# Kernel tuning notes

Measured on AMD Instinct MI355X. Metric: run time of the kernel, lower is better.

The kernel has to match this reference:

```python
import math
import jax, jax.numpy as jnp
import numpy as np

DIM = 256
B = 32
M = 2048
N = 2048


def setup_inputs() -> dict:
    key = jax.random.key(0)
    k1, k2, k3, k4 = jax.random.split(key, 4)
    query = jax.random.normal(k1, (B, DIM, M), dtype=jnp.float32)
    key_t = jax.random.normal(k2, (B, DIM, N), dtype=jnp.float32)
    value = jax.random.normal(k3, (B, DIM, N), dtype=jnp.float32)
    # orthogonal random projection via QR, as in the torch __init__
    proj = np.asarray(jax.random.normal(k4, (DIM, DIM), dtype=jnp.float32))
    orth_proj, _ = np.linalg.qr(proj)
    orth_proj = jnp.asarray(orth_proj, dtype=jnp.float32)
    return {"query": query, "key": key_t, "value": value, "orth_proj": orth_proj}


def reference(query, key, value, orth_proj):
    dim = orth_proj.shape[0]
    q = query / math.sqrt(dim)
    # kernel feature maps: relu(W^T x), channels-first layout b c m
    phi_q = jax.nn.relu(jnp.einsum('bcm,ce->bem', q, orth_proj))
    phi_k = jax.nn.relu(jnp.einsum('bcn,ce->ben', key, orth_proj))
    phi_k_rowsum = phi_k.sum(-1)                         # [b, e]
    scale = jnp.einsum('bem,be->bm', phi_q, phi_k_rowsum)  # [b, m]
    scale = 1.0 / (scale + 1e-8)
    phi_q = phi_q * scale[:, None, :]                    # [b, e, m]
    kv = jnp.einsum('ben,bdn->bed', phi_k, value)        # [b, e, d]
    out = jnp.einsum('bem,bed->bdm', phi_q, kv)          # [b, d, m]
    return out
```

## Files before the change

### kernel.cpp

```cpp
#include <hip/hip_runtime.h>

#define DIMC 256
#define BSZ  32
#define MDIM 2048
#define NDIM 2048

#define KVP_STRIDE ((size_t)BSZ * DIMC * DIMC)

typedef __attribute__((ext_vector_type(8))) short bf16x8;
typedef __attribute__((ext_vector_type(4))) float f32x4;

static __device__ __forceinline__ unsigned short f2bf(float x) {
  unsigned int u = __float_as_uint(x);
  u += 0x7fffu + ((u >> 16) & 1u);
  return (unsigned short)(u >> 16);
}
static __device__ __forceinline__ float bf2f(unsigned short h) {
  return __uint_as_float(((unsigned int)h) << 16);
}
static __device__ __forceinline__ unsigned int cvt_pk_bf16(float lo, float hi) {
  unsigned int r;
  asm("v_cvt_pk_bf16_f32 %0, %1, %2" : "=v"(r) : "v"(lo), "v"(hi));
  return r;
}

__global__ __launch_bounds__(256) void prep_kernel(
    const float* __restrict__ W, unsigned short* __restrict__ Wt,
    float* __restrict__ rowsum) {
  const int e = blockIdx.x, c = threadIdx.x;
  Wt[e * 256 + c] = f2bf(W[c * 256 + e]);
  if (e < 32) rowsum[e * 256 + c] = 0.f;
}

__global__ __launch_bounds__(256) void phi_kernel(
    const float* __restrict__ query, const float* __restrict__ key,
    const unsigned short* __restrict__ Wt,
    unsigned short* __restrict__ phi_q, unsigned short* __restrict__ phi_k,
    float* __restrict__ rowsum) {
  __shared__ unsigned short As[128 * 40];
  __shared__ unsigned short Bs[128 * 40];
  const int z = blockIdx.z;
  const bool isKey = z < BSZ;
  const int b = isKey ? z : z - BSZ;
  const int x0 = blockIdx.x * 128;
  const int e0 = blockIdx.y * 128;
  const int t = threadIdx.x;
  const int lane = t & 63, wave = t >> 6;
  const int wr = wave >> 1, wc = wave & 1;
  const int q = lane >> 4, l15 = lane & 15;
  const float* Xb =
      (isKey ? key : query) + (size_t)b * DIMC * NDIM;
  f32x4 acc[4][4];
#pragma unroll
  for (int i = 0; i < 4; ++i)
#pragma unroll
    for (int j = 0; j < 4; ++j) acc[i][j] = (f32x4){0.f, 0.f, 0.f, 0.f};

  const int arow = t >> 2, ac8 = (t & 3) << 3;
  const int xidx = t & 127, ch = (t >> 7) << 4;
  const float* src0 = Xb + (size_t)ch * NDIM + x0 + xidx;
  const unsigned short* wt0 = Wt + (size_t)(e0 + arow) * 256 + ac8;
  const unsigned short* wt1 = Wt + (size_t)(e0 + arow + 64) * 256 + ac8;

  float v[16];
#pragma unroll
  for (int i = 0; i < 16; ++i) v[i] = src0[(size_t)i * NDIM];
  uint4 w0 = *(const uint4*)wt0;
  uint4 w1 = *(const uint4*)wt1;

  for (int it = 0; it < 8; ++it) {
    const int k0 = it * 32;
    {
      unsigned int wpk[8];
#pragma unroll
      for (int i = 0; i < 8; ++i) wpk[i] = cvt_pk_bf16(v[2 * i], v[2 * i + 1]);
      *(uint4*)&Bs[xidx * 40 + ch] = *(const uint4*)&wpk[0];
      *(uint4*)&Bs[xidx * 40 + ch + 8] = *(const uint4*)&wpk[4];
      *(uint4*)&As[arow * 40 + ac8] = w0;
      *(uint4*)&As[(arow + 64) * 40 + ac8] = w1;
    }
    __syncthreads();
    if (it < 7) {
      const float* src = src0 + (size_t)(k0 + 32) * NDIM;
#pragma unroll
      for (int i = 0; i < 16; ++i) v[i] = src[(size_t)i * NDIM];
      w0 = *(const uint4*)(wt0 + k0 + 32);
      w1 = *(const uint4*)(wt1 + k0 + 32);
    }
    bf16x8 a[4], bv[4];
#pragma unroll
    for (int i = 0; i < 4; ++i)
      a[i] = *(const bf16x8*)&As[(wr * 64 + i * 16 + l15) * 40 + q * 8];
#pragma unroll
    for (int j = 0; j < 4; ++j)
      bv[j] = *(const bf16x8*)&Bs[(wc * 64 + j * 16 + l15) * 40 + q * 8];
#pragma unroll
    for (int i = 0; i < 4; ++i)
#pragma unroll
      for (int j = 0; j < 4; ++j)
        acc[i][j] =
            __builtin_amdgcn_mfma_f32_16x16x32_bf16(a[i], bv[j], acc[i][j], 0, 0, 0);
    __syncthreads();
  }

  if (isKey) {
    unsigned short* dst = phi_k + (size_t)b * DIMC * NDIM;
#pragma unroll
    for (int i = 0; i < 4; ++i)
#pragma unroll
      for (int r = 0; r < 4; ++r) {
        const int e = e0 + wr * 64 + i * 16 + q * 4 + r;
        float s = 0.f;
#pragma unroll
        for (int j = 0; j < 4; ++j) {
          float vv = acc[i][j][r];
          vv = vv > 0.f ? vv : 0.f;
          const int n = x0 + wc * 64 + j * 16 + l15;
          dst[(size_t)e * NDIM + n] = f2bf(vv);
          s += vv;
        }
#pragma unroll
        for (int m = 1; m < 16; m <<= 1) s += __shfl_xor(s, m, 64);
        if (l15 == 0) atomicAdd(&rowsum[b * DIMC + e], s);
      }
  } else {
    unsigned short* dst = phi_q + (size_t)b * MDIM * DIMC;
#pragma unroll
    for (int i = 0; i < 4; ++i) {
      const int ebase = e0 + wr * 64 + i * 16 + q * 4;
#pragma unroll
      for (int j = 0; j < 4; ++j) {
        const int m = x0 + wc * 64 + j * 16 + l15;
        float r0 = acc[i][j][0], r1 = acc[i][j][1];
        float r2 = acc[i][j][2], r3 = acc[i][j][3];
        r0 = r0 > 0.f ? r0 * 0.0625f : 0.f;
        r1 = r1 > 0.f ? r1 * 0.0625f : 0.f;
        r2 = r2 > 0.f ? r2 * 0.0625f : 0.f;
        r3 = r3 > 0.f ? r3 * 0.0625f : 0.f;
        uint2 p;
        p.x = cvt_pk_bf16(r0, r1);
        p.y = cvt_pk_bf16(r2, r3);
        *(uint2*)&dst[(size_t)m * DIMC + ebase] = p;
      }
    }
  }
}

__global__ __launch_bounds__(256) void kv_kernel(
    const float* __restrict__ value, const unsigned short* __restrict__ phi_k,
    unsigned short* __restrict__ kvp, int kshift) {
  __shared__ unsigned short As[128 * 72];
  __shared__ unsigned short Bs[128 * 72];
  const int b = blockIdx.z >> kshift, ks = blockIdx.z & ((1 << kshift) - 1);
  const int d0 = blockIdx.x * 128, e0 = blockIdx.y * 128;
  const int t = threadIdx.x;
  const int lane = t & 63, wave = t >> 6;
  const int wr = wave >> 1, wc = wave & 1;
  const int q = lane >> 4, l15 = lane & 15;
  f32x4 acc[4][4];
#pragma unroll
  for (int i = 0; i < 4; ++i)
#pragma unroll
    for (int j = 0; j < 4; ++j) acc[i][j] = (f32x4){0.f, 0.f, 0.f, 0.f};

  const int row = t >> 2;
  const int c4 = (t & 3) << 2;
  const int c8 = (t & 3) << 3;

  const float* asrc0 = value + ((size_t)b * DIMC + d0 + row) * NDIM;
  const float* asrc1 = asrc0 + (size_t)64 * NDIM;
  const unsigned short* bsrc0 = phi_k + ((size_t)b * DIMC + e0 + row) * NDIM;
  const unsigned short* bsrc1 = bsrc0 + (size_t)64 * NDIM;

  const int nchunk = NDIM >> kshift;
  const int nbeg = ks * nchunk;
  for (int n0 = nbeg; n0 < nbeg + nchunk; n0 += 64) {
    __syncthreads();
#pragma unroll
    for (int i = 0; i < 4; ++i) {
      float4 f0 = *(const float4*)(asrc0 + n0 + c4 + i * 16);
      float4 f1 = *(const float4*)(asrc1 + n0 + c4 + i * 16);
      uint2 w0, w1;
      w0.x = cvt_pk_bf16(f0.x, f0.y); w0.y = cvt_pk_bf16(f0.z, f0.w);
      w1.x = cvt_pk_bf16(f1.x, f1.y); w1.y = cvt_pk_bf16(f1.z, f1.w);
      *(uint2*)&As[row * 72 + c4 + i * 16] = w0;
      *(uint2*)&As[(row + 64) * 72 + c4 + i * 16] = w1;
    }
#pragma unroll
    for (int i = 0; i < 2; ++i) {
      uint4 p0 = *(const uint4*)(bsrc0 + n0 + c8 + i * 32);
      uint4 p1 = *(const uint4*)(bsrc1 + n0 + c8 + i * 32);
      *(uint4*)&Bs[row * 72 + c8 + i * 32] = p0;
      *(uint4*)&Bs[(row + 64) * 72 + c8 + i * 32] = p1;
    }
    __syncthreads();
#pragma unroll
    for (int kk = 0; kk < 64; kk += 32) {
      bf16x8 a[4], bv[4];
#pragma unroll
      for (int i = 0; i < 4; ++i)
        a[i] = *(const bf16x8*)&As[(wr * 64 + i * 16 + l15) * 72 + kk + q * 8];
#pragma unroll
      for (int j = 0; j < 4; ++j)
        bv[j] = *(const bf16x8*)&Bs[(wc * 64 + j * 16 + l15) * 72 + kk + q * 8];
#pragma unroll
      for (int i = 0; i < 4; ++i)
#pragma unroll
        for (int j = 0; j < 4; ++j)
          acc[i][j] = __builtin_amdgcn_mfma_f32_16x16x32_bf16(a[i], bv[j],
                                                              acc[i][j], 0, 0, 0);
    }
  }
  unsigned short* dst = kvp + (size_t)ks * KVP_STRIDE + (size_t)b * DIMC * DIMC;
#pragma unroll
  for (int i = 0; i < 4; ++i)
#pragma unroll
    for (int j = 0; j < 4; ++j) {
      const int e = e0 + wc * 64 + j * 16 + l15;
#pragma unroll
      for (int r = 0; r < 4; ++r) {
        const int d = d0 + wr * 64 + i * 16 + q * 4 + r;
        dst[(size_t)d * DIMC + e] = f2bf(acc[i][j][r]);
      }
    }
}

__global__ __launch_bounds__(256) void kvred_kernel(
    unsigned short* __restrict__ kvp, int KS) {
  const size_t idx8 = ((size_t)blockIdx.x * 256 + threadIdx.x) * 8;
  float s[8];
#pragma unroll
  for (int j = 0; j < 8; ++j) s[j] = 0.f;
  for (int p = 0; p < KS; ++p) {
    uint4 v = *(const uint4*)(kvp + (size_t)p * KVP_STRIDE + idx8);
    const unsigned short* u = (const unsigned short*)&v;
#pragma unroll
    for (int j = 0; j < 8; ++j) s[j] += bf2f(u[j]);
  }
  unsigned int w[4];
#pragma unroll
  for (int j = 0; j < 4; ++j) w[j] = cvt_pk_bf16(s[2 * j], s[2 * j + 1]);
  *(uint4*)(kvp + idx8) = *(const uint4*)w;
}

__global__ __launch_bounds__(256) void out_kernel(
    const unsigned short* __restrict__ kv,
    const unsigned short* __restrict__ phi_q,
    const float* __restrict__ rowsum, float* __restrict__ out) {
  __shared__ unsigned short As[128 * 40];
  __shared__ unsigned short Bs[128 * 40];
  __shared__ float rs_lds[256];
  __shared__ float red[512];
  __shared__ float scl[128];
  const int b = blockIdx.z;
  const int m0 = blockIdx.x * 128;
  const int d0 = blockIdx.y * 128;
  const int t = threadIdx.x;
  const int lane = t & 63, wave = t >> 6;
  const int wr = wave >> 1, wc = wave & 1;
  const int q = lane >> 4, l15 = lane & 15;

  rs_lds[t] = rowsum[b * DIMC + t];

  f32x4 acc[4][4];
#pragma unroll
  for (int i = 0; i < 4; ++i)
#pragma unroll
    for (int j = 0; j < 4; ++j) acc[i][j] = (f32x4){0.f, 0.f, 0.f, 0.f};

  const int row = t >> 2, c8 = (t & 3) << 3;
  const unsigned short* a0 = kv + ((size_t)b * DIMC + d0 + row) * DIMC + c8;
  const unsigned short* a1 = a0 + (size_t)64 * DIMC;
  const unsigned short* bsrc0 = phi_q + ((size_t)b * MDIM + m0 + row) * DIMC + c8;
  const unsigned short* bsrc1 = bsrc0 + (size_t)64 * DIMC;
  float sA = 0.f, sB = 0.f;

  uint4 pa0 = *(const uint4*)a0;
  uint4 pa1 = *(const uint4*)a1;
  uint4 pq0 = *(const uint4*)bsrc0;
  uint4 pq1 = *(const uint4*)bsrc1;

  for (int it = 0; it < 8; ++it) {
    const int k0 = it * 32;
    {
      *(uint4*)&As[row * 40 + c8] = pa0;
      *(uint4*)&As[(row + 64) * 40 + c8] = pa1;
      *(uint4*)&Bs[row * 40 + c8] = pq0;
      *(uint4*)&Bs[(row + 64) * 40 + c8] = pq1;
      const unsigned short* u0 = (const unsigned short*)&pq0;
      const unsigned short* u1 = (const unsigned short*)&pq1;
#pragma unroll
      for (int j = 0; j < 8; ++j) {
        const float r = rs_lds[k0 + c8 + j];
        sA += bf2f(u0[j]) * r;
        sB += bf2f(u1[j]) * r;
      }
    }
    __syncthreads();
    if (it < 7) {
      pa0 = *(const uint4*)(a0 + k0 + 32);
      pa1 = *(const uint4*)(a1 + k0 + 32);
      pq0 = *(const uint4*)(bsrc0 + k0 + 32);
      pq1 = *(const uint4*)(bsrc1 + k0 + 32);
    }
    bf16x8 a[4], bv[4];
#pragma unroll
    for (int i = 0; i < 4; ++i)
      a[i] = *(const bf16x8*)&As[(wr * 64 + i * 16 + l15) * 40 + q * 8];
#pragma unroll
    for (int j = 0; j < 4; ++j)
      bv[j] = *(const bf16x8*)&Bs[(wc * 64 + j * 16 + l15) * 40 + q * 8];
#pragma unroll
    for (int i = 0; i < 4; ++i)
#pragma unroll
      for (int j = 0; j < 4; ++j)
        acc[i][j] =
            __builtin_amdgcn_mfma_f32_16x16x32_bf16(a[i], bv[j], acc[i][j], 0, 0, 0);
    __syncthreads();
  }
  red[row * 4 + (t & 3)] = sA;
  red[(row + 64) * 4 + (t & 3)] = sB;
  __syncthreads();
  if (t < 128) {
    float s = red[t * 4] + red[t * 4 + 1] + red[t * 4 + 2] + red[t * 4 + 3];
    scl[t] = 1.f / (s + 1e-8f);
  }
  __syncthreads();

  float* ob = out + (size_t)b * DIMC * MDIM;
#pragma unroll
  for (int j = 0; j < 4; ++j) {
    const int ml = wc * 64 + j * 16 + l15;
    const int m = m0 + ml;
    const float sc = scl[ml];
#pragma unroll
    for (int i = 0; i < 4; ++i) {
#pragma unroll
      for (int r = 0; r < 4; ++r) {
        const int d = d0 + wr * 64 + i * 16 + q * 4 + r;
        ob[(size_t)d * MDIM + m] = acc[i][j][r] * sc;
      }
    }
  }
}

extern "C" void kernel_launch(void* const* d_in, const int* in_sizes, int n_in,
                              void* d_out, int out_size, void* d_ws, size_t ws_size,
                              hipStream_t stream) {
  const float* query = (const float*)d_in[0];
  const float* key   = (const float*)d_in[1];
  const float* value = (const float*)d_in[2];
  const float* W     = (const float*)d_in[3];
  float* out = (float*)d_out;

  unsigned short* Wt    = (unsigned short*)d_ws;
  unsigned short* phi_q = Wt + 65536;
  unsigned short* phi_k = phi_q + (size_t)BSZ * MDIM * DIMC;
  unsigned short* kvp   = phi_k + (size_t)BSZ * DIMC * NDIM;

  const size_t base_shorts =
      65536 + (size_t)BSZ * MDIM * DIMC + (size_t)BSZ * DIMC * NDIM;
  int KS = 8, kshift = 3;
  while (KS > 1 &&
         (base_shorts + (size_t)KS * KVP_STRIDE) * 2 + (size_t)BSZ * DIMC * 4 >
             ws_size) {
    KS >>= 1;
    kshift -= 1;
  }
  float* rowsum = (float*)(kvp + (size_t)KS * KVP_STRIDE);

  hipLaunchKernelGGL(prep_kernel, dim3(256), dim3(256), 0, stream, W, Wt, rowsum);
  hipLaunchKernelGGL(phi_kernel, dim3(MDIM / 128, DIMC / 128, BSZ * 2),
                     dim3(256), 0, stream, query, key, Wt, phi_q, phi_k, rowsum);
  hipLaunchKernelGGL(kv_kernel, dim3(DIMC / 128, DIMC / 128, BSZ << kshift),
                     dim3(256), 0, stream, value, phi_k, kvp, kshift);
  if (KS > 1)
    hipLaunchKernelGGL(kvred_kernel, dim3(1024), dim3(256), 0, stream, kvp, KS);
  hipLaunchKernelGGL(out_kernel, dim3(MDIM / 128, DIMC / 128, BSZ), dim3(256),
                     0, stream, kvp, phi_q, rowsum, out);
}
```

Before: 283.5 us.

## Double-buffer phi kernel LDS tiles with two-stage prefetch and float4 loads

Rewrites the phi feature-map GEMM main loop to use double-buffered shared memory tiles, keeping two stages of global loads in flight and committing the next tile while the current MFMAs run, with one barrier per iteration. Global reads of the input now use float4 vectors along the sequence dimension, and the LDS row stride changes from 40 to 36 halves with 8-byte fragment loads. The aim is to hide global load latency and cut barriers. In exchange it doubles LDS use and raises register pressure, which may reduce occupancy.

After: 278.0 us. About the same (-1.9%).

```diff
diff --git a/kernel.cpp b/kernel.cpp
--- a/kernel.cpp
+++ b/kernel.cpp
@@ -22,6 +22,13 @@
   unsigned int r;
   asm("v_cvt_pk_bf16_f32 %0, %1, %2" : "=v"(r) : "v"(lo), "v"(hi));
   return r;
+}
+static __device__ __forceinline__ bf16x8 ldfrag(const unsigned short* p) {
+  union { unsigned int u[4]; bf16x8 v; } r;
+  uint2 lo = *(const uint2*)p;
+  uint2 hi = *(const uint2*)(p + 4);
+  r.u[0] = lo.x; r.u[1] = lo.y; r.u[2] = hi.x; r.u[3] = hi.y;
+  return r.v;
 }
 
 __global__ __launch_bounds__(256) void prep_kernel(
@@ -37,71 +44,92 @@
     const unsigned short* __restrict__ Wt,
     unsigned short* __restrict__ phi_q, unsigned short* __restrict__ phi_k,
     float* __restrict__ rowsum) {
-  __shared__ unsigned short As[128 * 40];
-  __shared__ unsigned short Bs[128 * 40];
+  __shared__ unsigned short As[2][128 * 36];
+  __shared__ unsigned short Bs[2][128 * 36];
   const int z = blockIdx.z;
   const bool isKey = z < BSZ;
-  const int b = isKey ? z : z - BSZ;
+  const int b = z & (BSZ - 1);
   const int x0 = blockIdx.x * 128;
   const int e0 = blockIdx.y * 128;
   const int t = threadIdx.x;
   const int lane = t & 63, wave = t >> 6;
   const int wr = wave >> 1, wc = wave & 1;
   const int q = lane >> 4, l15 = lane & 15;
-  const float* Xb =
-      (isKey ? key : query) + (size_t)b * DIMC * NDIM;
+  const float* Xb = (isKey ? key : query) + (size_t)b * DIMC * NDIM;
+
   f32x4 acc[4][4];
 #pragma unroll
   for (int i = 0; i < 4; ++i)
 #pragma unroll
     for (int j = 0; j < 4; ++j) acc[i][j] = (f32x4){0.f, 0.f, 0.f, 0.f};
 
-  const int arow = t >> 2, ac8 = (t & 3) << 3;
-  const int xidx = t & 127, ch = (t >> 7) << 4;
-  const float* src0 = Xb + (size_t)ch * NDIM + x0 + xidx;
-  const unsigned short* wt0 = Wt + (size_t)(e0 + arow) * 256 + ac8;
-  const unsigned short* wt1 = Wt + (size_t)(e0 + arow + 64) * 256 + ac8;
-
-  float v[16];
-#pragma unroll
-  for (int i = 0; i < 16; ++i) v[i] = src0[(size_t)i * NDIM];
-  uint4 w0 = *(const uint4*)wt0;
-  uint4 w1 = *(const uint4*)wt1;
-
+  const int n4 = (t & 31) * 4, c4 = (t >> 5) * 4;
+  const int arow = t >> 2, ac8 = (t & 3) * 8;
+  const float* xsrc = Xb + (size_t)c4 * NDIM + x0 + n4;
+  const unsigned short* wtp = Wt + (size_t)(e0 + arow) * 256 + ac8;
+
+  float4 xf0[4], xf1[4];
+  uint4 wv0[2], wv1[2];
+
+#define PHI_ISSUE(xf, wv, k0_)                                          \
+  do {                                                                  \
+    _Pragma("unroll") for (int i = 0; i < 4; ++i)                       \
+        xf[i] = *(const float4*)(xsrc + (size_t)((k0_) + i) * NDIM);    \
+    wv[0] = *(const uint4*)(wtp + (k0_));                               \
+    wv[1] = *(const uint4*)(wtp + 64 * 256 + (k0_));                    \
+  } while (0)
+
+#define PHI_COMMIT(xf, wv, bufi)                                        \
+  do {                                                                  \
+    unsigned short* B_ = &Bs[bufi][0];                                  \
+    unsigned short* A_ = &As[bufi][0];                                  \
+    const float* fp = (const float*)&xf[0];                             \
+    _Pragma("unroll") for (int j = 0; j < 4; ++j) {                     \
+      uint2 p;                                                          \
+      p.x = cvt_pk_bf16(fp[0 * 4 + j], fp[1 * 4 + j]);                  \
+      p.y = cvt_pk_bf16(fp[2 * 4 + j], fp[3 * 4 + j]);                  \
+      *(uint2*)&B_[(n4 + j) * 36 + c4] = p;                             \
+    }                                                                   \
+    *(uint2*)&A_[arow * 36 + ac8] = make_uint2(wv[0].x, wv[0].y);       \
+    *(uint2*)&A_[arow * 36 + ac8 + 4] = make_uint2(wv[0].z, wv[0].w);   \
+    *(uint2*)&A_[(arow + 64) * 36 + ac8] = make_uint2(wv[1].x, wv[1].y);\
+    *(uint2*)&A_[(arow + 64) * 36 + ac8 + 4] =                          \
+        make_uint2(wv[1].z, wv[1].w);                                   \
+  } while (0)
+
+  PHI_ISSUE(xf0, wv0, 0);
+  PHI_ISSUE(xf1, wv1, 32);
+  PHI_COMMIT(xf0, wv0, 0);
+  __syncthreads();
+
+#pragma unroll
   for (int it = 0; it < 8; ++it) {
-    const int k0 = it * 32;
-    {
-      unsigned int wpk[8];
-#pragma unroll
-      for (int i = 0; i < 8; ++i) wpk[i] = cvt_pk_bf16(v[2 * i], v[2 * i + 1]);
-      *(uint4*)&Bs[xidx * 40 + ch] = *(const uint4*)&wpk[0];
-      *(uint4*)&Bs[xidx * 40 + ch + 8] = *(const uint4*)&wpk[4];
-      *(uint4*)&As[arow * 40 + ac8] = w0;
-      *(uint4*)&As[(arow + 64) * 40 + ac8] = w1;
-    }
-    __syncthreads();
-    if (it < 7) {
-      const float* src = src0 + (size_t)(k0 + 32) * NDIM;
-#pragma unroll
-      for (int i = 0; i < 16; ++i) v[i] = src[(size_t)i * NDIM];
-      w0 = *(const uint4*)(wt0 + k0 + 32);
-      w1 = *(const uint4*)(wt1 + k0 + 32);
-    }
+    const int cur = it & 1;
     bf16x8 a[4], bv[4];
 #pragma unroll
     for (int i = 0; i < 4; ++i)
-      a[i] = *(const bf16x8*)&As[(wr * 64 + i * 16 + l15) * 40 + q * 8];
+      a[i] = ldfrag(&As[cur][(wr * 64 + i * 16 + l15) * 36 + q * 8]);
 #pragma unroll
     for (int j = 0; j < 4; ++j)
-      bv[j] = *(const bf16x8*)&Bs[(wc * 64 + j * 16 + l15) * 40 + q * 8];
+      bv[j] = ldfrag(&Bs[cur][(wc * 64 + j * 16 + l15) * 36 + q * 8]);
+    if (it < 6) {
+      if (cur == 0) PHI_ISSUE(xf0, wv0, (it + 2) * 32);
+      else          PHI_ISSUE(xf1, wv1, (it + 2) * 32);
+    }
 #pragma unroll
     for (int i = 0; i < 4; ++i)
 #pragma unroll
       for (int j = 0; j < 4; ++j)
         acc[i][j] =
             __builtin_amdgcn_mfma_f32_16x16x32_bf16(a[i], bv[j], acc[i][j], 0, 0, 0);
+    if (it < 7) {
+      if (cur == 0) PHI_COMMIT(xf1, wv1, 1);
+      else          PHI_COMMIT(xf0, wv0, 0);
+    }
     __syncthreads();
   }
+#undef PHI_ISSUE
+#undef PHI_COMMIT
 
   if (isKey) {
     unsigned short* dst = phi_k + (size_t)b * DIMC * NDIM;
```
